# Kernel optimization log

Measured on AMD Instinct MI355X. Metric: run time of the kernel, lower is better.

## Reference

```python
import jax, jax.numpy as jnp
import numpy as np

ALPHA = 0.01  # leaky_relu slope (forward default)

def _hist_entropy(x, bins):
    """Mean over batch of per-sample histogram entropy, matching
    np.histogram(sample, bins=bins) + entropy_calc(hist, bw=bins):
      H = -sum(p*log(p)) - log(1/bins) = -sum(p*log(p)) + log(bins).
    x: [B, D] float."""
    B, D = x.shape
    xmin = jnp.min(x, axis=1, keepdims=True)
    xmax = jnp.max(x, axis=1, keepdims=True)
    width = xmax - xmin
    safe_w = jnp.where(width > 0, width, 1.0)
    # np.histogram: equal-width bins over [min, max]; max value goes in last bin
    idx = jnp.floor((x - xmin) / safe_w * bins).astype(jnp.int32)
    idx = jnp.clip(idx, 0, bins - 1)
    flat = (jnp.arange(B, dtype=jnp.int32)[:, None] * bins + idx).reshape(-1)
    counts = jnp.zeros(B * bins, jnp.float32).at[flat].add(1.0).reshape(B, bins)
    p = counts / jnp.float32(D)
    plogp = jnp.where(p > 0, p * jnp.log(jnp.where(p > 0, p, 1.0)), 0.0)
    H = -jnp.sum(plogp, axis=1) + jnp.log(jnp.float32(bins))  # [B]
    return jnp.mean(H)

def _lin(x, W, b):
    return x @ W.T + b

def setup_inputs() -> dict:
    key = jax.random.key(0)
    ks = jax.random.split(key, 13)
    B = 65536
    dims = [(784, 256), (256, 128), (128, 128), (128, 128), (128, 32), (32, 10)]
    inp = {"x": jax.random.normal(ks[0], (B, 784), dtype=jnp.float32)}
    for i, (din, dout) in enumerate(dims):
        s = 1.0 / np.sqrt(din)
        inp[f"W{i+1}"] = jax.random.uniform(ks[1 + 2 * i], (dout, din), jnp.float32, -s, s)
        inp[f"b{i+1}"] = jax.random.uniform(ks[2 + 2 * i], (dout,), jnp.float32, -s, s)
    return inp

def reference(x, W1, b1, W2, b2, W3, b3, W4, b4, W5, b5, W6, b6):
    x = x.reshape(-1, 784)
    Hs = []
    for (W, b) in [(W1, b1), (W2, b2), (W3, b3), (W4, b4), (W5, b5)]:
        x = jax.nn.leaky_relu(_lin(x, W, b), ALPHA)
        Hs.append(_hist_entropy(x, x.shape[1]))  # bins = dim / bin_ratio(=1)
    x = jax.nn.relu(_lin(x, W6, b6))
    out = jax.nn.log_softmax(x, axis=1)
    return (out, Hs[0], Hs[1], Hs[2], Hs[3], Hs[4])
```

## Files before the change

kernel.cpp:

```cpp
#include <hip/hip_runtime.h>
#include <hip/hip_bf16.h>
#include <math.h>

#define ALPHA 0.01f

typedef __bf16 bf16x8 __attribute__((ext_vector_type(8)));
typedef float  floatx4 __attribute__((ext_vector_type(4)));

static __device__ __forceinline__ unsigned short f2bf_bits(float f) {
    return __builtin_bit_cast(unsigned short, (__bf16)f);
}

template <int CTRL>
static __device__ __forceinline__ float dppmov(float x) {
    int r = __builtin_amdgcn_update_dpp(0, __builtin_bit_cast(int, x), CTRL, 0xf, 0xf, false);
    return __builtin_bit_cast(float, r);
}
static __device__ __forceinline__ float red16min(float x) {
    x = fminf(x, dppmov<0x121>(x)); x = fminf(x, dppmov<0x122>(x));
    x = fminf(x, dppmov<0x124>(x)); x = fminf(x, dppmov<0x128>(x));
    return x;
}
static __device__ __forceinline__ float red16max(float x) {
    x = fmaxf(x, dppmov<0x121>(x)); x = fmaxf(x, dppmov<0x122>(x));
    x = fmaxf(x, dppmov<0x124>(x)); x = fmaxf(x, dppmov<0x128>(x));
    return x;
}
static __device__ __forceinline__ float red16sum(float x) {
    x += dppmov<0x121>(x); x += dppmov<0x122>(x);
    x += dppmov<0x124>(x); x += dppmov<0x128>(x);
    return x;
}

static __device__ __forceinline__ uint4 pack8(float4 f0, float4 f1) {
    uint4 pk;
    pk.x = (unsigned)f2bf_bits(f0.x) | ((unsigned)f2bf_bits(f0.y) << 16);
    pk.y = (unsigned)f2bf_bits(f0.z) | ((unsigned)f2bf_bits(f0.w) << 16);
    pk.z = (unsigned)f2bf_bits(f1.x) | ((unsigned)f2bf_bits(f1.y) << 16);
    pk.w = (unsigned)f2bf_bits(f1.z) | ((unsigned)f2bf_bits(f1.w) << 16);
    return pk;
}

template <int DOUT>
static __device__ __forceinline__ float entropy_tile(const floatx4* acc,
        unsigned int* cc, int lane16)
{
    constexpr int CTN   = DOUT / 16;
    constexpr int HALF  = DOUT / 2;
    constexpr int LOG2D = (DOUT == 256) ? 8 : (DOUT == 128) ? 7 : 5;
    constexpr float LOGB = (DOUT == 256) ? 5.54517744f
                         : (DOUT == 128) ? 4.85203026f : 3.46573590f;
    float Hq = 0.0f;
    #pragma unroll
    for (int reg = 0; reg < 4; reg++) {
        float mn = acc[0][reg], mx = mn;
        #pragma unroll
        for (int ct = 1; ct < CTN; ct++) {
            mn = fminf(mn, acc[ct][reg]);
            mx = fmaxf(mx, acc[ct][reg]);
        }
        mn = red16min(mn);
        mx = red16max(mx);
        float wdt = mx - mn;
        float scale = (float)DOUT / (wdt > 0.0f ? wdt : 1.0f);

        #pragma unroll
        for (int i = 0; i < DOUT / 32; i++) cc[lane16 + 16 * i] = 0u;

        #pragma unroll
        for (int ct = 0; ct < CTN; ct++) {
            int b = (int)((acc[ct][reg] - mn) * scale);
            b = b < (DOUT - 1) ? b : (DOUT - 1);
            atomicAdd(&cc[b & (HALF - 1)],
                      1u << (((b >> (LOG2D - 1)) & 1) << 4));
        }

        float s = 0.0f;
        #pragma unroll
        for (int i = 0; i < DOUT / 32; i++) {
            unsigned int word = cc[lane16 + 16 * i];
            int c0 = (int)(word & 0xffffu), c1 = (int)(word >> 16);
            if (c0 > 0) { float p = (float)c0 * (1.0f / (float)DOUT); s += p * __logf(p); }
            if (c1 > 0) { float p = (float)c1 * (1.0f / (float)DOUT); s += p * __logf(p); }
        }
        s = red16sum(s);
        Hq += LOGB - s;
    }
    Hq += __shfl_xor(Hq, 16, 64);
    Hq += __shfl_xor(Hq, 32, 64);
    return Hq;
}

template <int DIN, int DOUT>
static __device__ __forceinline__ float tail_layer(const bf16x8* a,
    char* __restrict__ yt,
    const unsigned short* __restrict__ Wf, const float* __restrict__ bias,
    unsigned int* __restrict__ cc, int lane)
{
    constexpr int KT = DIN / 32, CTN = DOUT / 16, NCO = DOUT / 8;
    const int lane16 = lane & 15, q = lane >> 4;

    floatx4 acc[CTN];
    #pragma unroll
    for (int ct = 0; ct < CTN; ct++) acc[ct] = (floatx4)(bias[ct * 16 + lane16]);

    #pragma unroll
    for (int kt = 0; kt < KT; kt++) {
        #pragma unroll
        for (int ct = 0; ct < CTN; ct++) {
            bf16x8 bw = *(const bf16x8*)(Wf + ((size_t)(kt * CTN + ct) * 64 + lane) * 8);
            acc[ct] = __builtin_amdgcn_mfma_f32_16x16x32_bf16(a[kt], bw, acc[ct], 0, 0, 0);
        }
    }

    #pragma unroll
    for (int ct = 0; ct < CTN; ct++) {
        #pragma unroll
        for (int reg = 0; reg < 4; reg++) {
            float v = acc[ct][reg];
            v = v > 0.0f ? v : ALPHA * v;
            acc[ct][reg] = v;
            int r  = q * 4 + reg;
            int c  = (ct * 16 + lane16) >> 3;
            int cs = c ^ (r & (NCO - 1));
            *(unsigned short*)(yt + r * (DOUT * 2) + cs * 16 + (lane16 & 7) * 2)
                = f2bf_bits(v);
        }
    }
    return entropy_tile<DOUT>(acc, cc, lane16);
}

template <int DIN>
static __device__ __forceinline__ void load_afrags(bf16x8* a,
    const char* __restrict__ yt, int lane16, int q)
{
    constexpr int KT = DIN / 32, NCI = DIN / 8;
    asm volatile("s_waitcnt lgkmcnt(0)" ::: "memory");
    #pragma unroll
    for (int kt = 0; kt < KT; kt++) {
        int cs = (kt * 4 + q) ^ (lane16 & (NCI - 1));
        a[kt] = *(const bf16x8*)(yt + lane16 * (DIN * 2) + cs * 16);
    }
    asm volatile("s_waitcnt lgkmcnt(0)" ::: "memory");
}

__global__ __launch_bounds__(256, 4) void mega(
    const float* __restrict__ X,
    const unsigned short* __restrict__ W1f, const float* __restrict__ b1,
    const unsigned short* __restrict__ W2f, const float* __restrict__ b2,
    const unsigned short* __restrict__ W3f, const float* __restrict__ b3,
    const unsigned short* __restrict__ W4f, const float* __restrict__ b4,
    const unsigned short* __restrict__ W5f, const float* __restrict__ b5,
    const float* __restrict__ W6, const float* __restrict__ b6,
    float* __restrict__ out, float* __restrict__ Hpart)
{
    __shared__ __align__(16) char yts[4][4096];
    __shared__ unsigned int cnt[16][129];

    const int t = threadIdx.x;
    const int lane = t & 63, lane16 = lane & 15, q = lane >> 4, w = t >> 6;
    const int row0 = blockIdx.x * 64;
    const int myrow = w * 16 + lane16;
    unsigned int* cc = cnt[w * 4 + q];
    char* yt = yts[w];
    const int hidx = blockIdx.x * 4 + w;

    floatx4 acc1[16];
    #pragma unroll
    for (int ct = 0; ct < 16; ct++) acc1[ct] = (floatx4)(b1[ct * 16 + lane16]);
    {
        const float* Xr = X + (size_t)(row0 + myrow) * 784;
        float4 fa0 = *(const float4*)(Xr + q * 8);
        float4 fa1 = *(const float4*)(Xr + q * 8 + 4);
        #pragma unroll 1
        for (int kt = 0; kt < 24; kt++) {
            bf16x8 a = __builtin_bit_cast(bf16x8, pack8(fa0, fa1));
            int noff = (kt == 23) ? ((q & 1) * 8) : (q * 8);
            const float* nsrc = Xr + (kt + 1) * 32 + noff;
            fa0 = *(const float4*)(nsrc);
            fa1 = *(const float4*)(nsrc + 4);
            #pragma unroll
            for (int ct = 0; ct < 16; ct++) {
                bf16x8 bw = *(const bf16x8*)(W1f + ((size_t)(kt * 16 + ct) * 64 + lane) * 8);
                acc1[ct] = __builtin_amdgcn_mfma_f32_16x16x32_bf16(a, bw, acc1[ct], 0, 0, 0);
            }
        }
        uint4 pk = pack8(fa0, fa1);
        if (q >= 2) { pk.x = 0u; pk.y = 0u; pk.z = 0u; pk.w = 0u; }
        bf16x8 a = __builtin_bit_cast(bf16x8, pk);
        #pragma unroll
        for (int ct = 0; ct < 16; ct++) {
            bf16x8 bw = *(const bf16x8*)(W1f + ((size_t)(24 * 16 + ct) * 64 + lane) * 8);
            acc1[ct] = __builtin_amdgcn_mfma_f32_16x16x32_bf16(a, bw, acc1[ct], 0, 0, 0);
        }
    }

    #pragma unroll
    for (int ct = 0; ct < 16; ct++) {
        #pragma unroll
        for (int reg = 0; reg < 4; reg++) {
            float v = acc1[ct][reg];
            acc1[ct][reg] = v > 0.0f ? v : ALPHA * v;
        }
    }

    float H = entropy_tile<256>(acc1, cc, lane16);
    if (lane == 0) Hpart[0 * 4096 + hidx] = H;

    bf16x8 a2[8];
    #pragma unroll
    for (int p = 0; p < 2; p++) {
        #pragma unroll
        for (int ct = 0; ct < 8; ct++) {
            #pragma unroll
            for (int reg = 0; reg < 4; reg++) {
                int r  = q * 4 + reg;
                int c  = (ct * 16 + lane16) >> 3;
                int cs = c ^ r;
                *(unsigned short*)(yt + r * 256 + cs * 16 + (lane16 & 7) * 2)
                    = f2bf_bits(acc1[p * 8 + ct][reg]);
            }
        }
        asm volatile("s_waitcnt lgkmcnt(0)" ::: "memory");
        #pragma unroll
        for (int kt = 0; kt < 4; kt++) {
            int cs = (kt * 4 + q) ^ lane16;
            a2[p * 4 + kt] = *(const bf16x8*)(yt + lane16 * 256 + cs * 16);
        }
        asm volatile("s_waitcnt lgkmcnt(0)" ::: "memory");
    }

    H = tail_layer<256, 128>(a2, yt, W2f, b2, cc, lane);
    if (lane == 0) Hpart[1 * 4096 + hidx] = H;

    bf16x8 a[4];
    load_afrags<128>(a, yt, lane16, q);
    H = tail_layer<128, 128>(a, yt, W3f, b3, cc, lane);
    if (lane == 0) Hpart[2 * 4096 + hidx] = H;

    load_afrags<128>(a, yt, lane16, q);
    H = tail_layer<128, 128>(a, yt, W4f, b4, cc, lane);
    if (lane == 0) Hpart[3 * 4096 + hidx] = H;

    load_afrags<128>(a, yt, lane16, q);
    H = tail_layer<128, 32>(a, yt, W5f, b5, cc, lane);
    if (lane == 0) Hpart[4 * 4096 + hidx] = H;

    asm volatile("s_waitcnt lgkmcnt(0)" ::: "memory");
    float x6[32];
    #pragma unroll
    for (int c = 0; c < 4; c++) {
        int cs = c ^ (lane16 & 3);
        bf16x8 v = *(const bf16x8*)(yt + lane16 * 64 + cs * 16);
        #pragma unroll
        for (int j = 0; j < 8; j++) x6[c * 8 + j] = (float)v[j];
    }

    float z[3];
    float m = -1e30f;
    #pragma unroll
    for (int s2 = 0; s2 < 3; s2++) {
        int jj = q * 3 + s2;
        float a6 = 0.0f;
        if (jj < 10) {
            a6 = b6[jj];
            #pragma unroll
            for (int k = 0; k < 32; k++) a6 = fmaf(x6[k], W6[jj * 32 + k], a6);
            a6 = fmaxf(a6, 0.0f);
            m = fmaxf(m, a6);
        }
        z[s2] = a6;
    }
    m = fmaxf(m, __shfl_xor(m, 16, 64));
    m = fmaxf(m, __shfl_xor(m, 32, 64));
    float se = 0.0f;
    #pragma unroll
    for (int s2 = 0; s2 < 3; s2++)
        if (q * 3 + s2 < 10) se += __expf(z[s2] - m);
    se += __shfl_xor(se, 16, 64);
    se += __shfl_xor(se, 32, 64);
    float ls = __logf(se);
    const size_t ro = (size_t)(row0 + w * 16 + lane16) * 10;
    #pragma unroll
    for (int s2 = 0; s2 < 3; s2++) {
        int jj = q * 3 + s2;
        if (jj < 10) out[ro + jj] = z[s2] - m - ls;
    }
}

__global__ void convert_wfrag(const float* __restrict__ W1, const float* __restrict__ W2,
                              const float* __restrict__ W3, const float* __restrict__ W4,
                              const float* __restrict__ W5, unsigned short* __restrict__ out)
{
    int s = blockIdx.x * 256 + threadIdx.x;
    if (s >= 34304) return;
    const float* W; int DIN, CTN, sl;
    if      (s < 25600) { W = W1; DIN = 784; CTN = 16; sl = s;         }
    else if (s < 29696) { W = W2; DIN = 256; CTN = 8;  sl = s - 25600; }
    else if (s < 31744) { W = W3; DIN = 128; CTN = 8;  sl = s - 29696; }
    else if (s < 33792) { W = W4; DIN = 128; CTN = 8;  sl = s - 31744; }
    else                { W = W5; DIN = 128; CTN = 2;  sl = s - 33792; }
    int kt = sl / (CTN * 64);
    int ct = (sl / 64) % CTN;
    int ln = sl & 63;
    int r  = ct * 16 + (ln & 15);
    int k0 = kt * 32 + (ln >> 4) * 8;
    unsigned short v[8];
    #pragma unroll
    for (int j = 0; j < 8; j++) {
        int k = k0 + j;
        v[j] = (k < DIN) ? f2bf_bits(W[(size_t)r * DIN + k]) : (unsigned short)0;
    }
    uint4 pk;
    pk.x = (unsigned)v[0] | ((unsigned)v[1] << 16);
    pk.y = (unsigned)v[2] | ((unsigned)v[3] << 16);
    pk.z = (unsigned)v[4] | ((unsigned)v[5] << 16);
    pk.w = (unsigned)v[6] | ((unsigned)v[7] << 16);
    *(uint4*)(out + (size_t)s * 8) = pk;
}

__global__ __launch_bounds__(256) void hreduce(const float* __restrict__ Hp,
                                               float* __restrict__ out_tail)
{
    __shared__ float sm[4];
    const int t = threadIdx.x, lane = t & 63, w = t >> 6;
    const int l = blockIdx.x;
    const float* p = Hp + (size_t)l * 4096;
    float s = 0.0f;
    for (int i = t; i < 4096; i += 256) s += p[i];
    #pragma unroll
    for (int off = 1; off <= 32; off <<= 1) s += __shfl_xor(s, off, 64);
    if (lane == 0) sm[w] = s;
    __syncthreads();
    if (t == 0)
        out_tail[l] = (sm[0] + sm[1] + sm[2] + sm[3]) * (1.0f / 65536.0f);
}

extern "C" void kernel_launch(void* const* d_in, const int* in_sizes, int n_in,
                              void* d_out, int out_size, void* d_ws, size_t ws_size,
                              hipStream_t stream)
{
    const float* x  = (const float*)d_in[0];
    const float* W1 = (const float*)d_in[1];  const float* b1 = (const float*)d_in[2];
    const float* W2 = (const float*)d_in[3];  const float* b2 = (const float*)d_in[4];
    const float* W3 = (const float*)d_in[5];  const float* b3 = (const float*)d_in[6];
    const float* W4 = (const float*)d_in[7];  const float* b4 = (const float*)d_in[8];
    const float* W5 = (const float*)d_in[9];  const float* b5 = (const float*)d_in[10];
    const float* W6 = (const float*)d_in[11]; const float* b6 = (const float*)d_in[12];
    float* out = (float*)d_out;

    constexpr int B = 65536;
    char* ws = (char*)d_ws;
    float* Hpart = (float*)ws;
    unsigned short* Wfrag = (unsigned short*)(ws + 81920);
    unsigned short* W1f = Wfrag;
    unsigned short* W2f = W1f + 25600 * 8;
    unsigned short* W3f = W2f + 4096 * 8;
    unsigned short* W4f = W3f + 2048 * 8;
    unsigned short* W5f = W4f + 2048 * 8;

    convert_wfrag<<<134, 256, 0, stream>>>(W1, W2, W3, W4, W5, Wfrag);

    mega<<<B / 64, 256, 0, stream>>>(
        x, W1f, b1, W2f, b2, W3f, b3, W4f, b4, W5f, b5, W6, b6, out, Hpart);

    hreduce<<<5, 256, 0, stream>>>(Hpart, out + (size_t)B * 10);
}
```

Baseline: 408.2 us.

## Double-buffer W1 tiles in LDS via global_load_lds for layer-1 MFMA loop

Layer-1 weight fragments were previously read straight from global memory by every wave. They are now staged cooperatively into a 32KB LDS double buffer with direct global-to-LDS loads, so the next k-tile is fetched while the current one feeds the MFMAs. The yts and cnt scratch areas are aliased into the same region after the loop. This adds a block barrier every k-step and raises LDS use to 32KB, which may reduce occupancy under launch_bounds(256,4).

```diff
diff --git a/kernel.cpp b/kernel.cpp
--- a/kernel.cpp
+++ b/kernel.cpp
@@ -9,6 +9,12 @@
 
 static __device__ __forceinline__ unsigned short f2bf_bits(float f) {
     return __builtin_bit_cast(unsigned short, (__bf16)f);
+}
+
+static __device__ __forceinline__ void glds16(const void* g, void* l) {
+    __builtin_amdgcn_global_load_lds(
+        (const __attribute__((address_space(1))) unsigned int*)g,
+        (__attribute__((address_space(3))) unsigned int*)l, 16, 0, 0);
 }
 
 template <int CTRL>
@@ -154,46 +160,69 @@
     const float* __restrict__ W6, const float* __restrict__ b6,
     float* __restrict__ out, float* __restrict__ Hpart)
 {
-    __shared__ __align__(16) char yts[4][4096];
-    __shared__ unsigned int cnt[16][129];
+    __shared__ __align__(16) char region[32768];
 
     const int t = threadIdx.x;
     const int lane = t & 63, lane16 = lane & 15, q = lane >> 4, w = t >> 6;
     const int row0 = blockIdx.x * 64;
     const int myrow = w * 16 + lane16;
-    unsigned int* cc = cnt[w * 4 + q];
-    char* yt = yts[w];
     const int hidx = blockIdx.x * 4 + w;
 
     floatx4 acc1[16];
     #pragma unroll
     for (int ct = 0; ct < 16; ct++) acc1[ct] = (floatx4)(b1[ct * 16 + lane16]);
+
     {
+        auto stageW = [&](int kt2, char* buf) {
+            #pragma unroll
+            for (int i = 0; i < 4; i++)
+                glds16(W1f + ((size_t)kt2 * 1024 + w * 256 + i * 64 + lane) * 8,
+                       buf + (w * 256 + i * 64) * 16);
+        };
+
         const float* Xr = X + (size_t)(row0 + myrow) * 784;
+
+        stageW(0, region);
         float4 fa0 = *(const float4*)(Xr + q * 8);
         float4 fa1 = *(const float4*)(Xr + q * 8 + 4);
+        asm volatile("s_waitcnt vmcnt(0) lgkmcnt(0)" ::: "memory");
+        __builtin_amdgcn_s_barrier();
+
         #pragma unroll 1
         for (int kt = 0; kt < 24; kt++) {
+            char* bufC = region + ((kt & 1) << 14);
+            char* bufN = region + ((~kt & 1) << 14);
+            stageW(kt + 1, bufN);
+
             bf16x8 a = __builtin_bit_cast(bf16x8, pack8(fa0, fa1));
             int noff = (kt == 23) ? ((q & 1) * 8) : (q * 8);
             const float* nsrc = Xr + (kt + 1) * 32 + noff;
             fa0 = *(const float4*)(nsrc);
             fa1 = *(const float4*)(nsrc + 4);
+
             #pragma unroll
             for (int ct = 0; ct < 16; ct++) {
-                bf16x8 bw = *(const bf16x8*)(W1f + ((size_t)(kt * 16 + ct) * 64 + lane) * 8);
+                bf16x8 bw = *(const bf16x8*)(bufC + (ct * 64 + lane) * 16);
                 acc1[ct] = __builtin_amdgcn_mfma_f32_16x16x32_bf16(a, bw, acc1[ct], 0, 0, 0);
             }
-        }
+            asm volatile("s_waitcnt vmcnt(0) lgkmcnt(0)" ::: "memory");
+            __builtin_amdgcn_s_barrier();
+        }
+
         uint4 pk = pack8(fa0, fa1);
         if (q >= 2) { pk.x = 0u; pk.y = 0u; pk.z = 0u; pk.w = 0u; }
         bf16x8 a = __builtin_bit_cast(bf16x8, pk);
         #pragma unroll
         for (int ct = 0; ct < 16; ct++) {
-            bf16x8 bw = *(const bf16x8*)(W1f + ((size_t)(24 * 16 + ct) * 64 + lane) * 8);
+            bf16x8 bw = *(const bf16x8*)(region + (ct * 64 + lane) * 16);
             acc1[ct] = __builtin_amdgcn_mfma_f32_16x16x32_bf16(a, bw, acc1[ct], 0, 0, 0);
         }
-    }
+        asm volatile("s_waitcnt lgkmcnt(0)" ::: "memory");
+        __builtin_amdgcn_s_barrier();
+    }
+
+    char* yt = region + w * 4096;
+    unsigned int* cc = (unsigned int*)(region + 16384) + (w * 4 + q) * 129;
 
     #pragma unroll
     for (int ct = 0; ct < 16; ct++) {
```

New measurement: 390.1 us. -4.4%, faster.
